# Performance work log

Measured on AMD Instinct MI355X. Metric: run time of the kernel, lower is better.

## Reference

```python
import jax, jax.numpy as jnp
import numpy as np

N = 32768   # nodes
E = 32768   # edges
ND, ED, GD = 12, 5, 11
H = 64
T = 4
STEPS = 3


def setup_inputs() -> dict:
    key = jax.random.key(0)
    ks = jax.random.split(key, 24)
    s = 0.05
    p = lambda k, sh: (jax.random.normal(k, sh) * s).astype(jnp.float32)
    return dict(
        x=jax.random.normal(ks[0], (N, ND), jnp.float32),
        edge_index=jax.random.randint(ks[1], (2, E), 0, N, jnp.int64),
        edge_attr=jax.random.uniform(ks[2], (E, ED), jnp.float32),
        u=jax.random.normal(ks[3], (1, GD), jnp.float32),
        Wp=p(ks[4], (H, ND + GD)), bp=p(ks[5], (H,)),
        We1=p(ks[6], (H, ED)), be1=p(ks[7], (H,)),
        We2=p(ks[8], (H * H, H)), be2=p(ks[9], (H * H,)),
        root=p(ks[10], (H, H)), conv_b=p(ks[11], (H,)),
        Wih=p(ks[12], (3 * H, H)), bih=p(ks[13], (3 * H,)),
        Whh=p(ks[14], (3 * H, H)), bhh=p(ks[15], (3 * H,)),
        Wd1=p(ks[16], (H, 2 * H + ED)), bd1=p(ks[17], (H,)),
        Wd2=p(ks[18], (H // 2, H)), bd2=p(ks[19], (H // 2,)),
        Wd3=p(ks[20], (T, H // 2)), bd3=p(ks[21], (T,)),
    )


def _forward(x, edge_index, edge_attr, u,
             Wp, bp, We1, be1, We2, be2, root, conv_b,
             Wih, bih, Whh, bhh, Wd1, bd1, Wd2, bd2, Wd3, bd3):
    n = x.shape[0]
    e = edge_attr.shape[0]
    src, dst = edge_index[0], edge_index[1]

    # input projection with broadcast global features (batch=None path)
    u_node = jnp.broadcast_to(u, (n, u.shape[-1]))
    h = jnp.tanh(jnp.concatenate([x, u_node], axis=-1) @ Wp.T + bp)

    # edge MLP -> per-edge (H,H) weight matrices; edge_attr is loop-invariant
    ew = jax.nn.relu(edge_attr @ We1.T + be1) @ We2.T + be2   # (E, H*H)
    ew = ew.reshape(e, H, H)                                   # (E, H, H)

    # mean-aggregation denominators (clamped to 1 like scatter-mean)
    counts = jnp.clip(jax.ops.segment_sum(jnp.ones((e,), h.dtype), dst, num_segments=n), 1.0)

    for _ in range(STEPS):
        # NNConv: gather src features, per-edge matmul, scatter-mean into dst
        msg = jnp.einsum('eh,eho->eo', h[src], ew)             # (E, H)
        agg = jax.ops.segment_sum(msg, dst, num_segments=n) / counts[:, None]
        m = jax.nn.relu(agg + h @ root + conv_b)               # dropout off (eval)
        # GRUCell (torch gate order: r, z, n)
        gi = m @ Wih.T + bih
        gh = h @ Whh.T + bhh
        r = jax.nn.sigmoid(gi[:, :H] + gh[:, :H])
        z = jax.nn.sigmoid(gi[:, H:2 * H] + gh[:, H:2 * H])
        ng = jnp.tanh(gi[:, 2 * H:] + r * gh[:, 2 * H:])
        h = (1.0 - z) * ng + z * h

    # per-edge decoder
    e_in = jnp.concatenate([h[src], h[dst], edge_attr], axis=-1)
    d = jax.nn.relu(e_in @ Wd1.T + bd1)
    d = jax.nn.relu(d @ Wd2.T + bd2)
    return d @ Wd3.T + bd3                                     # (E, T)


def reference(x, edge_index, edge_attr, u,
              Wp, bp, We1, be1, We2, be2, root, conv_b,
              Wih, bih, Whh, bhh, Wd1, bd1, Wd2, bd2, Wd3, bd3):
    return _forward(x, edge_index, edge_attr, u,
                    Wp, bp, We1, be1, We2, be2, root, conv_b,
                    Wih, bih, Whh, bhh, Wd1, bd1, Wd2, bd2, Wd3, bd3)
```

## Files before the change

kernel.cpp:

```cpp
#include <hip/hip_runtime.h>
#include <hip/hip_bf16.h>
#include <stdint.h>


#define N_NODES 32768
#define N_EDGES 32768
#define STEPS 3

typedef __attribute__((ext_vector_type(8))) short short8;
typedef __attribute__((ext_vector_type(4))) float float4v;

__device__ __forceinline__ float bf2f(unsigned short u) {
    union { unsigned int i; float f; } v; v.i = ((unsigned int)u) << 16; return v.f;
}
__device__ __forceinline__ unsigned short f2bf(float f) {
    union { float f; unsigned int i; } v; v.f = f;
    unsigned int x = v.i;
    return (unsigned short)((x + 0x7fffu + ((x >> 16) & 1u)) >> 16);
}
__device__ __forceinline__ unsigned int fbits(float f) {
    union { float f; unsigned int i; } v; v.f = f; return v.i;
}

__device__ __forceinline__ short8 packA(float hv, const float* hf) {
    union { short8 v; unsigned int u[4]; } r;
#pragma unroll
    for (int p = 0; p < 4; p++) {
        unsigned int p0 = fbits(hv * hf[2 * p]) + 0x8000u;
        unsigned int p1 = fbits(hv * hf[2 * p + 1]) + 0x8000u;
        r.u[p] = __builtin_amdgcn_perm(p1, p0, 0x07060302u);
    }
    return r.v;
}

__device__ __forceinline__ void gload_lds16(const void* g, void* l) {
    __builtin_amdgcn_global_load_lds(
        (__attribute__((address_space(1))) void*)g,
        (__attribute__((address_space(3))) void*)l, 16, 0, 0);
}

__global__ __launch_bounds__(256) void k_setup(
    const float* __restrict__ root, const float* __restrict__ Wih,
    const float* __restrict__ Whh,
    const float* __restrict__ We2, const float* __restrict__ be2,
    const float* __restrict__ Wd1, const float* __restrict__ bd1,
    const float* __restrict__ Wd2,
    const float* __restrict__ x, const float* __restrict__ u,
    const float* __restrict__ Wp, const float* __restrict__ bp,
    const float* __restrict__ ea, const float* __restrict__ We1,
    const float* __restrict__ be1,
    unsigned short* __restrict__ rootTf, unsigned short* __restrict__ wcombf,
    unsigned short* __restrict__ w2tf,
    unsigned short* __restrict__ wd1f, unsigned short* __restrict__ wd2f,
    unsigned short* __restrict__ hb,
    unsigned short* __restrict__ hid, float* __restrict__ aggcnt)
{
    int b = blockIdx.x, tid = threadIdx.x;
    if (b < 144) {
        int i = b * 256 + tid;
        if (i < 4096) {
            int j = i & 7, lane = (i >> 3) & 63, g = i >> 9;
            int kb = g >> 2, nf = g & 3;
            int o = nf * 16 + (lane & 15);
            int k = kb * 32 + (lane >> 4) * 8 + j;
            rootTf[i] = f2bf(root[k * 64 + o]);
        } else if (i < 4096 + 32768) {
            int t = i - 4096;
            int j = t & 7, lane = (t >> 3) & 63, g = t >> 9;
            int kb = g >> 4, nf = g & 15;
            int cp = nf * 16 + (lane & 15);
            int k = kb * 32 + (lane >> 4) * 8 + j;
            float v;
            if (cp < 128)      v = (k < 64) ? Wih[cp * 64 + k] : Whh[cp * 64 + (k - 64)];
            else if (cp < 192) v = (k < 64) ? Wih[cp * 64 + k] : 0.f;
            else               v = (k < 64) ? 0.f : Whh[(cp - 64) * 64 + (k - 64)];
            wcombf[t] = f2bf(v);
        }
    } else if (b < 1184) {
        int t = (b - 144) * 256 + tid;
        if (t < 65 * 4096) {
            int kk = t >> 12, r = t & 4095;
            int j = r & 7, lane = (r >> 3) & 63, g = r >> 9;
            int half = g >> 2, nf = g & 3;
            int o = nf * 16 + (lane & 15);
            int hh = half * 32 + (lane >> 4) * 8 + j;
            float v = (kk < 64) ? We2[((size_t)(hh * 64 + o)) * 64 + kk]
                                : be2[(size_t)hh * 64 + o];
            w2tf[t] = f2bf(v);
        }
    } else if (b < 1232) {
        int i = (b - 1184) * 256 + tid;
        if (i < 10240) {
            int j = i & 7, lane = (i >> 3) & 63, g = i >> 9;
            int kb = g >> 2, nf = g & 3;
            int o = nf * 16 + (lane & 15);
            int k = kb * 32 + (lane >> 4) * 8 + j;
            float v = (k < 133) ? Wd1[(size_t)o * 133 + k] : (k == 133 ? bd1[o] : 0.f);
            wd1f[i] = f2bf(v);
        } else if (i < 10240 + 2048) {
            int t = i - 10240;
            int j = t & 7, lane = (t >> 3) & 63, g = t >> 9;
            int kb = g >> 1, nf = g & 1;
            int o = nf * 16 + (lane & 15);
            int k = kb * 32 + (lane >> 4) * 8 + j;
            wd2f[t] = f2bf(Wd2[(size_t)o * 64 + k]);
        }
    } else if (b < 9424) {
        int idx = (b - 1232) * 256 + tid;
        int n = idx >> 6, j = idx & 63;
        const float* wr = Wp + j * 23;
        const float* xr = x + (size_t)n * 12;
        float s = bp[j];
#pragma unroll
        for (int i = 0; i < 12; i++) s += xr[i] * wr[i];
#pragma unroll
        for (int i = 0; i < 11; i++) s += u[i] * wr[12 + i];
        hb[idx] = f2bf(tanhf(s));
    } else if (b < 17616) {
        int idx = (b - 9424) * 256 + tid;
        int e = idx >> 6, j = idx & 63;
        float s = be1[j];
#pragma unroll
        for (int i = 0; i < 5; i++) s += ea[(size_t)e * 5 + i] * We1[j * 5 + i];
        hid[idx] = f2bf(s > 0.f ? s : 0.f);
    } else {
        int idx = (b - 17616) * 1024 + tid * 4;
        if (idx < 2129920) {
            float4v z = {0.f, 0.f, 0.f, 0.f};
            *(float4v*)(aggcnt + idx) = z;
        }
    }
}

__global__ __launch_bounds__(256) void k_counts(
    const int* __restrict__ ei, float* __restrict__ counts)
{
    int i = blockIdx.x * 256 + threadIdx.x;
    if (i < N_EDGES) atomicAdd(&counts[ei[N_EDGES + i]], 1.0f);
}

__global__ __launch_bounds__(512, 4) void k_msg_fused(
    const unsigned short* __restrict__ hid,
    const unsigned short* __restrict__ hb,
    const unsigned short* __restrict__ w2tf,
    const int* __restrict__ ei,
    float* __restrict__ agg)
{
    __shared__ unsigned short buf[2][2][8192];
    int tid = threadIdx.x, wave = tid >> 6, lane = tid & 63;
    int l15 = lane & 15, quad = lane >> 4;
    int mf = wave & 3, kh = wave >> 2;
    int ebase = blockIdx.x * 64 + mf * 16;
    int e_a = ebase + l15;
    int src = ei[e_a];

    union { short8 v[4]; unsigned short u[32]; } hrow;
#pragma unroll
    for (int i = 0; i < 4; i++)
        hrow.v[i] = *(const short8*)(hid + (size_t)e_a * 64 + kh * 32 + i * 8);

    float hf0[8], hf1[8];
    {
        short8 h0 = *(const short8*)(hb + (size_t)src * 64 + quad * 8);
        short8 h1 = *(const short8*)(hb + (size_t)src * 64 + 32 + quad * 8);
#pragma unroll
        for (int j = 0; j < 8; j++) {
            hf0[j] = bf2f((unsigned short)h0[j]);
            hf1[j] = bf2f((unsigned short)h1[j]);
        }
    }

    int kk0 = kh ? 32 : 0;
    auto stage = [&](int pair, int db) {
        const unsigned short* g = w2tf + (size_t)(kk0 + 2 * pair) * 4096;
#pragma unroll
        for (int c = 0; c < 4; c++) {
            int chunk = mf * 4 + c;
            gload_lds16(g + (size_t)chunk * 512 + lane * 8, &buf[kh][db][chunk * 512]);
        }
    };

    stage(0, 0);

    float4v acc[4] = {};
    int cur = 0;
#pragma unroll
    for (int i = 0; i <= 16; i++) {
        __syncthreads();
        if ((kh == 0 && i + 1 < 16) || (kh == 1 && i + 1 <= 16))
            stage(i + 1, cur ^ 1);
        int nkk = (kh == 0) ? (i < 16 ? 2 : 0) : (i < 16 ? 2 : 1);
        for (int s = 0; s < nkk; s++) {
            float hv = (kh == 1 && i == 16) ? 1.0f : bf2f(hrow.u[2 * i + s]);
            short8 a0 = packA(hv, hf0);
            short8 a1 = packA(hv, hf1);
            const unsigned short* bp = &buf[kh][cur][s * 4096];
#pragma unroll
            for (int nf = 0; nf < 4; nf++) {
                short8 b0 = *(const short8*)(bp + (0 * 4 + nf) * 512 + lane * 8);
                acc[nf] = __builtin_amdgcn_mfma_f32_16x16x32_bf16(a0, b0, acc[nf], 0, 0, 0);
            }
#pragma unroll
            for (int nf = 0; nf < 4; nf++) {
                short8 b1 = *(const short8*)(bp + (1 * 4 + nf) * 512 + lane * 8);
                acc[nf] = __builtin_amdgcn_mfma_f32_16x16x32_bf16(a1, b1, acc[nf], 0, 0, 0);
            }
        }
        cur ^= 1;
    }

    __syncthreads();
    float* mg = (float*)&buf[0][0][0];
    if (kh == 1) {
#pragma unroll
        for (int nf = 0; nf < 4; nf++)
#pragma unroll
            for (int r = 0; r < 4; r++)
                mg[mf * 1024 + lane * 16 + nf * 4 + r] = acc[nf][r];
    }
    __syncthreads();
    if (kh == 0) {
        int dsts[4];
#pragma unroll
        for (int r = 0; r < 4; r++) dsts[r] = ei[N_EDGES + ebase + quad * 4 + r];
#pragma unroll
        for (int nf = 0; nf < 4; nf++)
#pragma unroll
            for (int r = 0; r < 4; r++)
                atomicAdd(agg + (size_t)dsts[r] * 64 + nf * 16 + l15,
                          acc[nf][r] + mg[mf * 1024 + lane * 16 + nf * 4 + r]);
    }
}

__global__ __launch_bounds__(256) void k_node(
    const unsigned short* __restrict__ hb_in,
    const unsigned short* __restrict__ rootTf,
    const unsigned short* __restrict__ wcombf,
    float* __restrict__ agg, const float* __restrict__ counts,
    const float* __restrict__ conv_b,
    const float* __restrict__ bih, const float* __restrict__ bhh,
    unsigned short* __restrict__ hb_out)
{
    __shared__ unsigned short m_lds[64 * 72];
    int tid = threadIdx.x, w = tid >> 6, lane = tid & 63;
    int l15 = lane & 15, quad = lane >> 4;
    int node0 = blockIdx.x * 64;
    int row0 = w * 16;

    float4v acc1[4] = {};
    {
        short8 a1[2];
#pragma unroll
        for (int kb = 0; kb < 2; kb++)
            a1[kb] = *(const short8*)(hb_in + (size_t)(node0 + row0 + l15) * 64 + kb * 32 + quad * 8);
#pragma unroll
        for (int kb = 0; kb < 2; kb++)
#pragma unroll
            for (int nf = 0; nf < 4; nf++) {
                short8 b = *(const short8*)(rootTf + (size_t)((kb * 4 + nf) * 64 + lane) * 8);
                acc1[nf] = __builtin_amdgcn_mfma_f32_16x16x32_bf16(a1[kb], b, acc1[nf], 0, 0, 0);
            }
    }
#pragma unroll
    for (int rr = 0; rr < 4; rr++) {
        int nl = row0 + quad * 4 + rr;
        float cnt = counts[node0 + nl]; if (cnt < 1.f) cnt = 1.f;
        float rcp = 1.f / cnt;
#pragma unroll
        for (int nf = 0; nf < 4; nf++) {
            int c = nf * 16 + l15;
            float* ap = agg + (size_t)(node0 + nl) * 64 + c;
            float av = *ap;
            *ap = 0.f;
            float mv = av * rcp + acc1[nf][rr] + conv_b[c];
            m_lds[nl * 72 + c] = f2bf(mv > 0.f ? mv : 0.f);
        }
    }
    __syncthreads();

    float4v acc2[16] = {};
#pragma unroll
    for (int kb = 0; kb < 4; kb++) {
        short8 a2;
        if (kb < 2)
            a2 = *(const short8*)(m_lds + (row0 + l15) * 72 + kb * 32 + quad * 8);
        else
            a2 = *(const short8*)(hb_in + (size_t)(node0 + row0 + l15) * 64 + (kb - 2) * 32 + quad * 8);
#pragma unroll
        for (int nf = 0; nf < 16; nf++) {
            short8 b = *(const short8*)(wcombf + (size_t)((kb * 16 + nf) * 64 + lane) * 8);
            acc2[nf] = __builtin_amdgcn_mfma_f32_16x16x32_bf16(a2, b, acc2[nf], 0, 0, 0);
        }
    }

#pragma unroll
    for (int nf0 = 0; nf0 < 4; nf0++) {
        int c = nf0 * 16 + l15;
        float br = bih[c] + bhh[c];
        float bz = bih[64 + c] + bhh[64 + c];
        float bni = bih[128 + c], bnh = bhh[128 + c];
#pragma unroll
        for (int rr = 0; rr < 4; rr++) {
            int node = node0 + row0 + quad * 4 + rr;
            float gr = 1.f / (1.f + __expf(-(acc2[nf0][rr] + br)));
            float gz = 1.f / (1.f + __expf(-(acc2[nf0 + 4][rr] + bz)));
            float ng = tanhf(acc2[nf0 + 8][rr] + bni + gr * (acc2[nf0 + 12][rr] + bnh));
            float ho = bf2f(hb_in[(size_t)node * 64 + c]);
            float hn = (1.f - gz) * ng + gz * ho;
            hb_out[(size_t)node * 64 + c] = f2bf(hn);
        }
    }
}

__global__ __launch_bounds__(256) void k_decoder(
    const unsigned short* __restrict__ hb, const int* __restrict__ ei,
    const float* __restrict__ ea,
    const unsigned short* __restrict__ wd1f, const unsigned short* __restrict__ wd2f,
    const float* __restrict__ bd2,
    const float* __restrict__ Wd3, const float* __restrict__ bd3,
    float* __restrict__ out)
{
    __shared__ unsigned short d1f[4][1024];
    __shared__ float d2s[4][16 * 33];
    int tid = threadIdx.x, w = tid >> 6, lane = tid & 63;
    int l15 = lane & 15, quad = lane >> 4;
    int ebase = blockIdx.x * 64 + w * 16;
    int e = ebase + l15;
    int src = ei[e], dst = ei[N_EDGES + e];

    short8 a[5];
#pragma unroll
    for (int kb = 0; kb < 2; kb++) {
        a[kb]     = *(const short8*)(hb + (size_t)src * 64 + kb * 32 + quad * 8);
        a[2 + kb] = *(const short8*)(hb + (size_t)dst * 64 + kb * 32 + quad * 8);
    }
    {
        union { short8 v; unsigned short u[8]; } tea;
#pragma unroll
        for (int j = 0; j < 8; j++) {
            float vv = 0.f;
            if (quad == 0) vv = (j < 5) ? ea[(size_t)e * 5 + j] : (j == 5 ? 1.f : 0.f);
            tea.u[j] = f2bf(vv);
        }
        a[4] = tea.v;
    }

    float4v acc1[4] = {};
#pragma unroll
    for (int kb = 0; kb < 5; kb++)
#pragma unroll
        for (int nf = 0; nf < 4; nf++) {
            short8 b = *(const short8*)(wd1f + (size_t)((kb * 4 + nf) * 64 + lane) * 8);
            acc1[nf] = __builtin_amdgcn_mfma_f32_16x16x32_bf16(a[kb], b, acc1[nf], 0, 0, 0);
        }
#pragma unroll
    for (int nf = 0; nf < 4; nf++) {
        int kbp = nf >> 1;
        int lanep_hi = ((nf & 1) * 2 + (l15 >> 3)) * 16;
        int jp = l15 & 7;
#pragma unroll
        for (int r = 0; r < 4; r++) {
            float v = acc1[nf][r];
            d1f[w][kbp * 512 + (lanep_hi + quad * 4 + r) * 8 + jp] = f2bf(v > 0.f ? v : 0.f);
        }
    }
    float4v acc2[2] = {};
#pragma unroll
    for (int kb = 0; kb < 2; kb++) {
        short8 a2 = *(const short8*)(&d1f[w][kb * 512 + lane * 8]);
#pragma unroll
        for (int nf = 0; nf < 2; nf++) {
            short8 b = *(const short8*)(wd2f + (size_t)((kb * 2 + nf) * 64 + lane) * 8);
            acc2[nf] = __builtin_amdgcn_mfma_f32_16x16x32_bf16(a2, b, acc2[nf], 0, 0, 0);
        }
    }
#pragma unroll
    for (int nf = 0; nf < 2; nf++) {
        int c = nf * 16 + l15;
        float bias = bd2[c];
#pragma unroll
        for (int r = 0; r < 4; r++) {
            float v = acc2[nf][r] + bias;
            d2s[w][(quad * 4 + r) * 33 + c] = v > 0.f ? v : 0.f;
        }
    }
    {
        int e_l = lane >> 2, t = lane & 3;
        float s = bd3[t];
        const float* w3 = Wd3 + t * 32;
        const float* dr = &d2s[w][e_l * 33];
#pragma unroll
        for (int k = 0; k < 32; k++) s += w3[k] * dr[k];
        out[(size_t)(ebase + e_l) * 4 + t] = s;
    }
}

extern "C" void kernel_launch(void* const* d_in, const int* in_sizes, int n_in,
                              void* d_out, int out_size, void* d_ws, size_t ws_size,
                              hipStream_t stream)
{
    const float* x      = (const float*)d_in[0];
    const int*   ei     = (const int*)d_in[1];
    const float* ea     = (const float*)d_in[2];
    const float* u      = (const float*)d_in[3];
    const float* Wp     = (const float*)d_in[4];
    const float* bp     = (const float*)d_in[5];
    const float* We1    = (const float*)d_in[6];
    const float* be1    = (const float*)d_in[7];
    const float* We2    = (const float*)d_in[8];
    const float* be2    = (const float*)d_in[9];
    const float* root   = (const float*)d_in[10];
    const float* conv_b = (const float*)d_in[11];
    const float* Wih    = (const float*)d_in[12];
    const float* bih    = (const float*)d_in[13];
    const float* Whh    = (const float*)d_in[14];
    const float* bhh    = (const float*)d_in[15];
    const float* Wd1    = (const float*)d_in[16];
    const float* bd1    = (const float*)d_in[17];
    const float* Wd2    = (const float*)d_in[18];
    const float* bd2    = (const float*)d_in[19];
    const float* Wd3    = (const float*)d_in[20];
    const float* bd3    = (const float*)d_in[21];
    float* out = (float*)d_out;

    char* ws = (char*)d_ws;
    size_t off = 0;
    auto take = [&](size_t bytes) -> char* {
        char* p = ws + off; off = (off + bytes + 255) & ~(size_t)255; return p;
    };
    unsigned short* hb     = (unsigned short*)take((size_t)N_NODES * 64 * 2);
    unsigned short* hid    = (unsigned short*)take((size_t)N_EDGES * 64 * 2);
    float*          aggcnt = (float*)take((size_t)(N_NODES * 64 + N_NODES) * 4);
    float*          agg    = aggcnt;
    float*          cnts   = aggcnt + (size_t)N_NODES * 64;
    unsigned short* w2tf   = (unsigned short*)take((size_t)66 * 4096 * 2);
    unsigned short* rootTf = (unsigned short*)take((size_t)4096 * 2);
    unsigned short* wcombf = (unsigned short*)take((size_t)32768 * 2);
    unsigned short* wd1f   = (unsigned short*)take((size_t)10240 * 2);
    unsigned short* wd2f   = (unsigned short*)take((size_t)2048 * 2);
    (void)ws_size;

    k_setup<<<19696, 256, 0, stream>>>(root, Wih, Whh, We2, be2, Wd1, bd1, Wd2,
                                       x, u, Wp, bp, ea, We1, be1,
                                       rootTf, wcombf, w2tf, wd1f, wd2f,
                                       hb, hid, aggcnt);
    k_counts<<<128, 256, 0, stream>>>(ei, cnts);

    for (int s = 0; s < STEPS; s++) {
        k_msg_fused<<<N_EDGES / 64, 512, 0, stream>>>(hid, hb, w2tf, ei, agg);
        k_node<<<N_NODES / 64, 256, 0, stream>>>(hb, rootTf, wcombf, agg, cnts,
                                                 conv_b, bih, bhh, hb);
    }
    k_decoder<<<N_EDGES / 64, 256, 0, stream>>>(hb, ei, ea, wd1f, wd2f, bd2,
                                                Wd3, bd3, out);
}
```

Baseline: 267.0 us.

## Fuse counts, message steps, node updates and decoder into one cooperative kernel

Replaces the separate counts, per-step message, node-update and decoder launches with one persistent cooperative kernel of 256 blocks. Grid-wide syncs separate the phases. Each block now handles 128 edges or nodes, and each wave processes two 16-edge fragments that share the staged edge-weight tiles. This cuts kernel launch gaps and halves weight staging per edge. In exchange, only one 512-thread block runs per CU, which lowers occupancy and latency hiding, and each step adds grid-sync costs.

After: 981.0 us. 267% more time.

```diff
diff --git a/kernel.cpp b/kernel.cpp
--- a/kernel.cpp
+++ b/kernel.cpp
@@ -1,4 +1,5 @@
 #include <hip/hip_runtime.h>
+#include <hip/hip_cooperative_groups.h>
 #include <hip/hip_bf16.h>
 #include <stdint.h>
 
@@ -6,6 +7,8 @@
 #define N_NODES 32768
 #define N_EDGES 32768
 #define STEPS 3
+
+namespace cg = cooperative_groups;
 
 typedef __attribute__((ext_vector_type(8))) short short8;
 typedef __attribute__((ext_vector_type(4))) float float4v;
@@ -132,266 +135,277 @@
     }
 }
 
-__global__ __launch_bounds__(256) void k_counts(
-    const int* __restrict__ ei, float* __restrict__ counts)
-{
-    int i = blockIdx.x * 256 + threadIdx.x;
-    if (i < N_EDGES) atomicAdd(&counts[ei[N_EDGES + i]], 1.0f);
-}
-
-__global__ __launch_bounds__(512, 4) void k_msg_fused(
+__global__ __launch_bounds__(512, 2) void k_main(
     const unsigned short* __restrict__ hid,
-    const unsigned short* __restrict__ hb,
+    unsigned short* __restrict__ hb,
     const unsigned short* __restrict__ w2tf,
     const int* __restrict__ ei,
-    float* __restrict__ agg)
-{
-    __shared__ unsigned short buf[2][2][8192];
-    int tid = threadIdx.x, wave = tid >> 6, lane = tid & 63;
-    int l15 = lane & 15, quad = lane >> 4;
-    int mf = wave & 3, kh = wave >> 2;
-    int ebase = blockIdx.x * 64 + mf * 16;
-    int e_a = ebase + l15;
-    int src = ei[e_a];
-
-    union { short8 v[4]; unsigned short u[32]; } hrow;
-#pragma unroll
-    for (int i = 0; i < 4; i++)
-        hrow.v[i] = *(const short8*)(hid + (size_t)e_a * 64 + kh * 32 + i * 8);
-
-    float hf0[8], hf1[8];
-    {
-        short8 h0 = *(const short8*)(hb + (size_t)src * 64 + quad * 8);
-        short8 h1 = *(const short8*)(hb + (size_t)src * 64 + 32 + quad * 8);
-#pragma unroll
-        for (int j = 0; j < 8; j++) {
-            hf0[j] = bf2f((unsigned short)h0[j]);
-            hf1[j] = bf2f((unsigned short)h1[j]);
-        }
-    }
-
-    int kk0 = kh ? 32 : 0;
-    auto stage = [&](int pair, int db) {
-        const unsigned short* g = w2tf + (size_t)(kk0 + 2 * pair) * 4096;
-#pragma unroll
-        for (int c = 0; c < 4; c++) {
-            int chunk = mf * 4 + c;
-            gload_lds16(g + (size_t)chunk * 512 + lane * 8, &buf[kh][db][chunk * 512]);
-        }
-    };
-
-    stage(0, 0);
-
-    float4v acc[4] = {};
-    int cur = 0;
-#pragma unroll
-    for (int i = 0; i <= 16; i++) {
-        __syncthreads();
-        if ((kh == 0 && i + 1 < 16) || (kh == 1 && i + 1 <= 16))
-            stage(i + 1, cur ^ 1);
-        int nkk = (kh == 0) ? (i < 16 ? 2 : 0) : (i < 16 ? 2 : 1);
-        for (int s = 0; s < nkk; s++) {
-            float hv = (kh == 1 && i == 16) ? 1.0f : bf2f(hrow.u[2 * i + s]);
-            short8 a0 = packA(hv, hf0);
-            short8 a1 = packA(hv, hf1);
-            const unsigned short* bp = &buf[kh][cur][s * 4096];
-#pragma unroll
-            for (int nf = 0; nf < 4; nf++) {
-                short8 b0 = *(const short8*)(bp + (0 * 4 + nf) * 512 + lane * 8);
-                acc[nf] = __builtin_amdgcn_mfma_f32_16x16x32_bf16(a0, b0, acc[nf], 0, 0, 0);
-            }
-#pragma unroll
-            for (int nf = 0; nf < 4; nf++) {
-                short8 b1 = *(const short8*)(bp + (1 * 4 + nf) * 512 + lane * 8);
-                acc[nf] = __builtin_amdgcn_mfma_f32_16x16x32_bf16(a1, b1, acc[nf], 0, 0, 0);
-            }
-        }
-        cur ^= 1;
-    }
-
-    __syncthreads();
-    float* mg = (float*)&buf[0][0][0];
-    if (kh == 1) {
-#pragma unroll
-        for (int nf = 0; nf < 4; nf++)
-#pragma unroll
-            for (int r = 0; r < 4; r++)
-                mg[mf * 1024 + lane * 16 + nf * 4 + r] = acc[nf][r];
-    }
-    __syncthreads();
-    if (kh == 0) {
-        int dsts[4];
-#pragma unroll
-        for (int r = 0; r < 4; r++) dsts[r] = ei[N_EDGES + ebase + quad * 4 + r];
-#pragma unroll
-        for (int nf = 0; nf < 4; nf++)
-#pragma unroll
-            for (int r = 0; r < 4; r++)
-                atomicAdd(agg + (size_t)dsts[r] * 64 + nf * 16 + l15,
-                          acc[nf][r] + mg[mf * 1024 + lane * 16 + nf * 4 + r]);
-    }
-}
-
-__global__ __launch_bounds__(256) void k_node(
-    const unsigned short* __restrict__ hb_in,
+    float* __restrict__ agg, float* __restrict__ cnts,
     const unsigned short* __restrict__ rootTf,
     const unsigned short* __restrict__ wcombf,
-    float* __restrict__ agg, const float* __restrict__ counts,
     const float* __restrict__ conv_b,
     const float* __restrict__ bih, const float* __restrict__ bhh,
-    unsigned short* __restrict__ hb_out)
-{
-    __shared__ unsigned short m_lds[64 * 72];
-    int tid = threadIdx.x, w = tid >> 6, lane = tid & 63;
-    int l15 = lane & 15, quad = lane >> 4;
-    int node0 = blockIdx.x * 64;
-    int row0 = w * 16;
-
-    float4v acc1[4] = {};
-    {
-        short8 a1[2];
-#pragma unroll
-        for (int kb = 0; kb < 2; kb++)
-            a1[kb] = *(const short8*)(hb_in + (size_t)(node0 + row0 + l15) * 64 + kb * 32 + quad * 8);
-#pragma unroll
-        for (int kb = 0; kb < 2; kb++)
-#pragma unroll
-            for (int nf = 0; nf < 4; nf++) {
-                short8 b = *(const short8*)(rootTf + (size_t)((kb * 4 + nf) * 64 + lane) * 8);
-                acc1[nf] = __builtin_amdgcn_mfma_f32_16x16x32_bf16(a1[kb], b, acc1[nf], 0, 0, 0);
-            }
-    }
-#pragma unroll
-    for (int rr = 0; rr < 4; rr++) {
-        int nl = row0 + quad * 4 + rr;
-        float cnt = counts[node0 + nl]; if (cnt < 1.f) cnt = 1.f;
-        float rcp = 1.f / cnt;
-#pragma unroll
-        for (int nf = 0; nf < 4; nf++) {
-            int c = nf * 16 + l15;
-            float* ap = agg + (size_t)(node0 + nl) * 64 + c;
-            float av = *ap;
-            *ap = 0.f;
-            float mv = av * rcp + acc1[nf][rr] + conv_b[c];
-            m_lds[nl * 72 + c] = f2bf(mv > 0.f ? mv : 0.f);
-        }
-    }
-    __syncthreads();
-
-    float4v acc2[16] = {};
-#pragma unroll
-    for (int kb = 0; kb < 4; kb++) {
-        short8 a2;
-        if (kb < 2)
-            a2 = *(const short8*)(m_lds + (row0 + l15) * 72 + kb * 32 + quad * 8);
-        else
-            a2 = *(const short8*)(hb_in + (size_t)(node0 + row0 + l15) * 64 + (kb - 2) * 32 + quad * 8);
-#pragma unroll
-        for (int nf = 0; nf < 16; nf++) {
-            short8 b = *(const short8*)(wcombf + (size_t)((kb * 16 + nf) * 64 + lane) * 8);
-            acc2[nf] = __builtin_amdgcn_mfma_f32_16x16x32_bf16(a2, b, acc2[nf], 0, 0, 0);
-        }
-    }
-
-#pragma unroll
-    for (int nf0 = 0; nf0 < 4; nf0++) {
-        int c = nf0 * 16 + l15;
-        float br = bih[c] + bhh[c];
-        float bz = bih[64 + c] + bhh[64 + c];
-        float bni = bih[128 + c], bnh = bhh[128 + c];
-#pragma unroll
-        for (int rr = 0; rr < 4; rr++) {
-            int node = node0 + row0 + quad * 4 + rr;
-            float gr = 1.f / (1.f + __expf(-(acc2[nf0][rr] + br)));
-            float gz = 1.f / (1.f + __expf(-(acc2[nf0 + 4][rr] + bz)));
-            float ng = tanhf(acc2[nf0 + 8][rr] + bni + gr * (acc2[nf0 + 12][rr] + bnh));
-            float ho = bf2f(hb_in[(size_t)node * 64 + c]);
-            float hn = (1.f - gz) * ng + gz * ho;
-            hb_out[(size_t)node * 64 + c] = f2bf(hn);
-        }
-    }
-}
-
-__global__ __launch_bounds__(256) void k_decoder(
-    const unsigned short* __restrict__ hb, const int* __restrict__ ei,
     const float* __restrict__ ea,
-    const unsigned short* __restrict__ wd1f, const unsigned short* __restrict__ wd2f,
+    const unsigned short* __restrict__ wd1f,
+    const unsigned short* __restrict__ wd2f,
     const float* __restrict__ bd2,
     const float* __restrict__ Wd3, const float* __restrict__ bd3,
     float* __restrict__ out)
 {
-    __shared__ unsigned short d1f[4][1024];
-    __shared__ float d2s[4][16 * 33];
-    int tid = threadIdx.x, w = tid >> 6, lane = tid & 63;
+    cg::grid_group grid = cg::this_grid();
+    __shared__ unsigned short smem[2][2][8192];
+    int tid = threadIdx.x, wave = tid >> 6, lane = tid & 63;
     int l15 = lane & 15, quad = lane >> 4;
-    int ebase = blockIdx.x * 64 + w * 16;
-    int e = ebase + l15;
-    int src = ei[e], dst = ei[N_EDGES + e];
-
-    short8 a[5];
-#pragma unroll
-    for (int kb = 0; kb < 2; kb++) {
-        a[kb]     = *(const short8*)(hb + (size_t)src * 64 + kb * 32 + quad * 8);
-        a[2 + kb] = *(const short8*)(hb + (size_t)dst * 64 + kb * 32 + quad * 8);
+
+    {
+        int gtid = blockIdx.x * 512 + tid;
+        if (gtid < N_EDGES) atomicAdd(&cnts[ei[N_EDGES + gtid]], 1.0f);
     }
+
+    for (int step = 0; step < STEPS; step++) {
+        {
+            int mf = wave & 3, kh = wave >> 2;
+            int ebase = blockIdx.x * 128 + mf * 32;
+            int src0 = ei[ebase + l15], src1 = ei[ebase + 16 + l15];
+
+            union Hrow { short8 v[4]; unsigned short u[32]; };
+            Hrow hrow[2];
+#pragma unroll
+            for (int i = 0; i < 4; i++) {
+                hrow[0].v[i] = *(const short8*)(hid + (size_t)(ebase + l15) * 64 + kh * 32 + i * 8);
+                hrow[1].v[i] = *(const short8*)(hid + (size_t)(ebase + 16 + l15) * 64 + kh * 32 + i * 8);
+            }
+            float hf[2][2][8];
+#pragma unroll
+            for (int f = 0; f < 2; f++) {
+                int src = f ? src1 : src0;
+                short8 h0 = *(const short8*)(hb + (size_t)src * 64 + quad * 8);
+                short8 h1 = *(const short8*)(hb + (size_t)src * 64 + 32 + quad * 8);
+#pragma unroll
+                for (int j = 0; j < 8; j++) {
+                    hf[f][0][j] = bf2f((unsigned short)h0[j]);
+                    hf[f][1][j] = bf2f((unsigned short)h1[j]);
+                }
+            }
+
+            int kk0 = kh ? 32 : 0;
+            auto stage = [&](int pair, int db) {
+                const unsigned short* g = w2tf + (size_t)(kk0 + 2 * pair) * 4096;
+#pragma unroll
+                for (int c = 0; c < 4; c++) {
+                    int chunk = mf * 4 + c;
+                    gload_lds16(g + (size_t)chunk * 512 + lane * 8, &smem[kh][db][chunk * 512]);
+                }
+            };
+            stage(0, 0);
+
+            float4v acc[2][4] = {};
+            int cur = 0;
+#pragma unroll
+            for (int i = 0; i <= 16; i++) {
+                __syncthreads();
+                if ((kh == 0 && i + 1 < 16) || (kh == 1 && i + 1 <= 16))
+                    stage(i + 1, cur ^ 1);
+                int nkk = (kh == 0) ? (i < 16 ? 2 : 0) : (i < 16 ? 2 : 1);
+                for (int s = 0; s < nkk; s++) {
+                    const unsigned short* bp = &smem[kh][cur][s * 4096];
+                    short8 b0[4], b1[4];
+#pragma unroll
+                    for (int nf = 0; nf < 4; nf++) {
+                        b0[nf] = *(const short8*)(bp + (0 * 4 + nf) * 512 + lane * 8);
+                        b1[nf] = *(const short8*)(bp + (1 * 4 + nf) * 512 + lane * 8);
+                    }
+#pragma unroll
+                    for (int f = 0; f < 2; f++) {
+                        float hv = (kh == 1 && i == 16) ? 1.0f : bf2f(hrow[f].u[2 * i + s]);
+                        short8 a0 = packA(hv, hf[f][0]);
+                        short8 a1 = packA(hv, hf[f][1]);
+#pragma unroll
+                        for (int nf = 0; nf < 4; nf++)
+                            acc[f][nf] = __builtin_amdgcn_mfma_f32_16x16x32_bf16(a0, b0[nf], acc[f][nf], 0, 0, 0);
+#pragma unroll
+                        for (int nf = 0; nf < 4; nf++)
+                            acc[f][nf] = __builtin_amdgcn_mfma_f32_16x16x32_bf16(a1, b1[nf], acc[f][nf], 0, 0, 0);
+                    }
+                }
+                cur ^= 1;
+            }
+
+            __syncthreads();
+            float* mg = (float*)&smem[0][0][0];
+            if (kh == 1) {
+#pragma unroll
+                for (int f = 0; f < 2; f++)
+#pragma unroll
+                    for (int nf = 0; nf < 4; nf++)
+#pragma unroll
+                        for (int r = 0; r < 4; r++)
+                            mg[(mf * 2 + f) * 1024 + lane * 16 + nf * 4 + r] = acc[f][nf][r];
+            }
+            __syncthreads();
+            if (kh == 0) {
+#pragma unroll
+                for (int f = 0; f < 2; f++) {
+                    int dsts[4];
+#pragma unroll
+                    for (int r = 0; r < 4; r++)
+                        dsts[r] = ei[N_EDGES + ebase + f * 16 + quad * 4 + r];
+#pragma unroll
+                    for (int nf = 0; nf < 4; nf++)
+#pragma unroll
+                        for (int r = 0; r < 4; r++)
+                            atomicAdd(agg + (size_t)dsts[r] * 64 + nf * 16 + l15,
+                                      acc[f][nf][r] + mg[(mf * 2 + f) * 1024 + lane * 16 + nf * 4 + r]);
+                }
+            }
+        }
+        __threadfence();
+        grid.sync();
+
+        {
+            unsigned short* m_lds = (unsigned short*)&smem[0][0][0];
+            int node0 = blockIdx.x * 128;
+            int row0 = wave * 16;
+
+            float4v acc1[4] = {};
+            {
+                short8 a1[2];
+#pragma unroll
+                for (int kb = 0; kb < 2; kb++)
+                    a1[kb] = *(const short8*)(hb + (size_t)(node0 + row0 + l15) * 64 + kb * 32 + quad * 8);
+#pragma unroll
+                for (int kb = 0; kb < 2; kb++)
+#pragma unroll
+                    for (int nf = 0; nf < 4; nf++) {
+                        short8 b = *(const short8*)(rootTf + (size_t)((kb * 4 + nf) * 64 + lane) * 8);
+                        acc1[nf] = __builtin_amdgcn_mfma_f32_16x16x32_bf16(a1[kb], b, acc1[nf], 0, 0, 0);
+                    }
+            }
+#pragma unroll
+            for (int rr = 0; rr < 4; rr++) {
+                int nl = row0 + quad * 4 + rr;
+                float cnt = cnts[node0 + nl]; if (cnt < 1.f) cnt = 1.f;
+                float rcp = 1.f / cnt;
+#pragma unroll
+                for (int nf = 0; nf < 4; nf++) {
+                    int c = nf * 16 + l15;
+                    float* ap = agg + (size_t)(node0 + nl) * 64 + c;
+                    float av = *ap;
+                    *ap = 0.f;
+                    float mv = av * rcp + acc1[nf][rr] + conv_b[c];
+                    m_lds[nl * 72 + c] = f2bf(mv > 0.f ? mv : 0.f);
+                }
+            }
+            __syncthreads();
+
+            float4v acc2[16] = {};
+#pragma unroll
+            for (int kb = 0; kb < 4; kb++) {
+                short8 a2;
+                if (kb < 2)
+                    a2 = *(const short8*)(m_lds + (row0 + l15) * 72 + kb * 32 + quad * 8);
+                else
+                    a2 = *(const short8*)(hb + (size_t)(node0 + row0 + l15) * 64 + (kb - 2) * 32 + quad * 8);
+#pragma unroll
+                for (int nf = 0; nf < 16; nf++) {
+                    short8 b = *(const short8*)(wcombf + (size_t)((kb * 16 + nf) * 64 + lane) * 8);
+                    acc2[nf] = __builtin_amdgcn_mfma_f32_16x16x32_bf16(a2, b, acc2[nf], 0, 0, 0);
+                }
+            }
+#pragma unroll
+            for (int nf0 = 0; nf0 < 4; nf0++) {
+                int c = nf0 * 16 + l15;
+                float br = bih[c] + bhh[c];
+                float bz = bih[64 + c] + bhh[64 + c];
+                float bni = bih[128 + c], bnh = bhh[128 + c];
+#pragma unroll
+                for (int rr = 0; rr < 4; rr++) {
+                    int node = node0 + row0 + quad * 4 + rr;
+                    float gr = 1.f / (1.f + __expf(-(acc2[nf0][rr] + br)));
+                    float gz = 1.f / (1.f + __expf(-(acc2[nf0 + 4][rr] + bz)));
+                    float ng = tanhf(acc2[nf0 + 8][rr] + bni + gr * (acc2[nf0 + 12][rr] + bnh));
+                    float ho = bf2f(hb[(size_t)node * 64 + c]);
+                    float hn = (1.f - gz) * ng + gz * ho;
+                    hb[(size_t)node * 64 + c] = f2bf(hn);
+                }
+            }
+        }
+        __threadfence();
+        grid.sync();
+    }
+
     {
-        union { short8 v; unsigned short u[8]; } tea;
-#pragma unroll
-        for (int j = 0; j < 8; j++) {
-            float vv = 0.f;
-            if (quad == 0) vv = (j < 5) ? ea[(size_t)e * 5 + j] : (j == 5 ? 1.f : 0.f);
-            tea.u[j] = f2bf(vv);
-        }
-        a[4] = tea.v;
-    }
-
-    float4v acc1[4] = {};
-#pragma unroll
-    for (int kb = 0; kb < 5; kb++)
+        unsigned short* d1f = (unsigned short*)&smem[0][0][0];
+        float* d2s = (float*)((char*)&smem[0][0][0] + 16384);
+        int ebase = blockIdx.x * 128 + wave * 16;
+        int e = ebase + l15;
+        int src = ei[e], dst = ei[N_EDGES + e];
+
+        short8 a[5];
+#pragma unroll
+        for (int kb = 0; kb < 2; kb++) {
+            a[kb]     = *(const short8*)(hb + (size_t)src * 64 + kb * 32 + quad * 8);
+            a[2 + kb] = *(const short8*)(hb + (size_t)dst * 64 + kb * 32 + quad * 8);
+        }
+        {
+            union { short8 v; unsigned short u[8]; } tea;
+#pragma unroll
+            for (int j = 0; j < 8; j++) {
+                float vv = 0.f;
+                if (quad == 0) vv = (j < 5) ? ea[(size_t)e * 5 + j] : (j == 5 ? 1.f : 0.f);
+                tea.u[j] = f2bf(vv);
+            }
+            a[4] = tea.v;
+        }
+
+        float4v acc1[4] = {};
+#pragma unroll
+        for (int kb = 0; kb < 5; kb++)
+#pragma unroll
+            for (int nf = 0; nf < 4; nf++) {
+                short8 b = *(const short8*)(wd1f + (size_t)((kb * 4 + nf) * 64 + lane) * 8);
+                acc1[nf] = __builtin_amdgcn_mfma_f32_16x16x32_bf16(a[kb], b, acc1[nf], 0, 0, 0);
+            }
 #pragma unroll
         for (int nf = 0; nf < 4; nf++) {
-            short8 b = *(const short8*)(wd1f + (size_t)((kb * 4 + nf) * 64 + lane) * 8);
-            acc1[nf] = __builtin_amdgcn_mfma_f32_16x16x32_bf16(a[kb], b, acc1[nf], 0, 0, 0);
-        }
-#pragma unroll
-    for (int nf = 0; nf < 4; nf++) {
-        int kbp = nf >> 1;
-        int lanep_hi = ((nf & 1) * 2 + (l15 >> 3)) * 16;
-        int jp = l15 & 7;
-#pragma unroll
-        for (int r = 0; r < 4; r++) {
-            float v = acc1[nf][r];
-            d1f[w][kbp * 512 + (lanep_hi + quad * 4 + r) * 8 + jp] = f2bf(v > 0.f ? v : 0.f);
-        }
-    }
-    float4v acc2[2] = {};
-#pragma unroll
-    for (int kb = 0; kb < 2; kb++) {
-        short8 a2 = *(const short8*)(&d1f[w][kb * 512 + lane * 8]);
+            int kbp = nf >> 1;
+            int lanep_hi = ((nf & 1) * 2 + (l15 >> 3)) * 16;
+            int jp = l15 & 7;
+#pragma unroll
+            for (int r = 0; r < 4; r++) {
+                float v = acc1[nf][r];
+                d1f[wave * 1024 + kbp * 512 + (lanep_hi + quad * 4 + r) * 8 + jp] = f2bf(v > 0.f ? v : 0.f);
+            }
+        }
+        float4v acc2[2] = {};
+#pragma unroll
+        for (int kb = 0; kb < 2; kb++) {
+            short8 a2 = *(const short8*)(&d1f[wave * 1024 + kb * 512 + lane * 8]);
+#pragma unroll
+            for (int nf = 0; nf < 2; nf++) {
+                short8 b = *(const short8*)(wd2f + (size_t)((kb * 2 + nf) * 64 + lane) * 8);
+                acc2[nf] = __builtin_amdgcn_mfma_f32_16x16x32_bf16(a2, b, acc2[nf], 0, 0, 0);
+            }
+        }
 #pragma unroll
         for (int nf = 0; nf < 2; nf++) {
-            short8 b = *(const short8*)(wd2f + (size_t)((kb * 2 + nf) * 64 + lane) * 8);
-            acc2[nf] = __builtin_amdgcn_mfma_f32_16x16x32_bf16(a2, b, acc2[nf], 0, 0, 0);
-        }
-    }
-#pragma unroll
-    for (int nf = 0; nf < 2; nf++) {
-        int c = nf * 16 + l15;
-        float bias = bd2[c];
-#pragma unroll
-        for (int r = 0; r < 4; r++) {
-            float v = acc2[nf][r] + bias;
-            d2s[w][(quad * 4 + r) * 33 + c] = v > 0.f ? v : 0.f;
-        }
-    }
-    {
-        int e_l = lane >> 2, t = lane & 3;
-        float s = bd3[t];
-        const float* w3 = Wd3 + t * 32;
-        const float* dr = &d2s[w][e_l * 33];
-#pragma unroll
-        for (int k = 0; k < 32; k++) s += w3[k] * dr[k];
-        out[(size_t)(ebase + e_l) * 4 + t] = s;
+            int c = nf * 16 + l15;
+            float bias = bd2[c];
+#pragma unroll
+            for (int r = 0; r < 4; r++) {
+                float v = acc2[nf][r] + bias;
+                d2s[wave * 528 + (quad * 4 + r) * 33 + c] = v > 0.f ? v : 0.f;
+            }
+        }
+        {
+            int e_l = lane >> 2, t = lane & 3;
+            float s = bd3[t];
+            const float* w3 = Wd3 + t * 32;
+            const float* dr = &d2s[wave * 528 + e_l * 33];
+#pragma unroll
+            for (int k = 0; k < 32; k++) s += w3[k] * dr[k];
+            out[(size_t)(ebase + e_l) * 4 + t] = s;
+        }
     }
 }
 
@@ -444,13 +458,14 @@
                                        x, u, Wp, bp, ea, We1, be1,
                                        rootTf, wcombf, w2tf, wd1f, wd2f,
                                        hb, hid, aggcnt);
-    k_counts<<<128, 256, 0, stream>>>(ei, cnts);
-
-    for (int s = 0; s < STEPS; s++) {
-        k_msg_fused<<<N_EDGES / 64, 512, 0, stream>>>(hid, hb, w2tf, ei, agg);
-        k_node<<<N_NODES / 64, 256, 0, stream>>>(hb, rootTf, wcombf, agg, cnts,
-                                                 conv_b, bih, bhh, hb);
-    }
-    k_decoder<<<N_EDGES / 64, 256, 0, stream>>>(hb, ei, ea, wd1f, wd2f, bd2,
-                                                Wd3, bd3, out);
-}
+
+    void* args[] = {
+        (void*)&hid, (void*)&hb, (void*)&w2tf, (void*)&ei,
+        (void*)&agg, (void*)&cnts, (void*)&rootTf, (void*)&wcombf,
+        (void*)&conv_b, (void*)&bih, (void*)&bhh, (void*)&ea,
+        (void*)&wd1f, (void*)&wd2f, (void*)&bd2,
+        (void*)&Wd3, (void*)&bd3, (void*)&out
+    };
+    hipLaunchCooperativeKernel((const void*)k_main, dim3(256), dim3(512),
+                               args, 0, stream);
+}
```

## Give each message wave two 16-edge tiles to reuse staged weight fragments

Applied to the files above, without the earlier changes.

The message kernel drops from 8 waves to 4 per block, and each wave now computes two 16-edge M-fragments. Each LDS-loaded B fragment of the edge-network weight therefore feeds twice as many MFMAs, halving LDS read traffic per MFMA. Each wave also stages twice as many weight chunks. The partial-sum exchange buffer is padded with stride 17 to reduce bank conflicts. The cost is more registers per wave (two accumulator sets, more h buffers) and fewer waves per block, which may reduce latency hiding; the main k loop is also no longer fully unrolled.

After: 332.8 us. 1.25x slower.

```diff
diff --git a/kernel.cpp b/kernel.cpp
--- a/kernel.cpp
+++ b/kernel.cpp
@@ -139,7 +139,7 @@
     if (i < N_EDGES) atomicAdd(&counts[ei[N_EDGES + i]], 1.0f);
 }
 
-__global__ __launch_bounds__(512, 4) void k_msg_fused(
+__global__ __launch_bounds__(256) void k_msg_fused(
     const unsigned short* __restrict__ hid,
     const unsigned short* __restrict__ hb,
     const unsigned short* __restrict__ w2tf,
@@ -149,24 +149,25 @@
     __shared__ unsigned short buf[2][2][8192];
     int tid = threadIdx.x, wave = tid >> 6, lane = tid & 63;
     int l15 = lane & 15, quad = lane >> 4;
-    int mf = wave & 3, kh = wave >> 2;
-    int ebase = blockIdx.x * 64 + mf * 16;
-    int e_a = ebase + l15;
-    int src = ei[e_a];
-
-    union { short8 v[4]; unsigned short u[32]; } hrow;
-#pragma unroll
-    for (int i = 0; i < 4; i++)
-        hrow.v[i] = *(const short8*)(hid + (size_t)e_a * 64 + kh * 32 + i * 8);
-
-    float hf0[8], hf1[8];
-    {
+    int mf = wave & 1, kh = wave >> 1;
+    int ebase = blockIdx.x * 64 + mf * 32;
+
+    union Hrow { short8 v[4]; unsigned short u[32]; };
+    Hrow hrow[2];
+    float hf[2][2][8];
+#pragma unroll
+    for (int f = 0; f < 2; f++) {
+        int e_a = ebase + f * 16 + l15;
+#pragma unroll
+        for (int i = 0; i < 4; i++)
+            hrow[f].v[i] = *(const short8*)(hid + (size_t)e_a * 64 + kh * 32 + i * 8);
+        int src = ei[e_a];
         short8 h0 = *(const short8*)(hb + (size_t)src * 64 + quad * 8);
         short8 h1 = *(const short8*)(hb + (size_t)src * 64 + 32 + quad * 8);
 #pragma unroll
         for (int j = 0; j < 8; j++) {
-            hf0[j] = bf2f((unsigned short)h0[j]);
-            hf1[j] = bf2f((unsigned short)h1[j]);
+            hf[f][0][j] = bf2f((unsigned short)h0[j]);
+            hf[f][1][j] = bf2f((unsigned short)h1[j]);
         }
     }
 
@@ -174,36 +175,39 @@
     auto stage = [&](int pair, int db) {
         const unsigned short* g = w2tf + (size_t)(kk0 + 2 * pair) * 4096;
 #pragma unroll
-        for (int c = 0; c < 4; c++) {
-            int chunk = mf * 4 + c;
+        for (int c = 0; c < 8; c++) {
+            int chunk = mf * 8 + c;
             gload_lds16(g + (size_t)chunk * 512 + lane * 8, &buf[kh][db][chunk * 512]);
         }
     };
-
     stage(0, 0);
 
-    float4v acc[4] = {};
+    float4v acc[2][4] = {};
     int cur = 0;
-#pragma unroll
     for (int i = 0; i <= 16; i++) {
         __syncthreads();
         if ((kh == 0 && i + 1 < 16) || (kh == 1 && i + 1 <= 16))
             stage(i + 1, cur ^ 1);
         int nkk = (kh == 0) ? (i < 16 ? 2 : 0) : (i < 16 ? 2 : 1);
         for (int s = 0; s < nkk; s++) {
-            float hv = (kh == 1 && i == 16) ? 1.0f : bf2f(hrow.u[2 * i + s]);
-            short8 a0 = packA(hv, hf0);
-            short8 a1 = packA(hv, hf1);
             const unsigned short* bp = &buf[kh][cur][s * 4096];
+            short8 b0[4], b1[4];
 #pragma unroll
             for (int nf = 0; nf < 4; nf++) {
-                short8 b0 = *(const short8*)(bp + (0 * 4 + nf) * 512 + lane * 8);
-                acc[nf] = __builtin_amdgcn_mfma_f32_16x16x32_bf16(a0, b0, acc[nf], 0, 0, 0);
+                b0[nf] = *(const short8*)(bp + (0 * 4 + nf) * 512 + lane * 8);
+                b1[nf] = *(const short8*)(bp + (1 * 4 + nf) * 512 + lane * 8);
             }
 #pragma unroll
-            for (int nf = 0; nf < 4; nf++) {
-                short8 b1 = *(const short8*)(bp + (1 * 4 + nf) * 512 + lane * 8);
-                acc[nf] = __builtin_amdgcn_mfma_f32_16x16x32_bf16(a1, b1, acc[nf], 0, 0, 0);
+            for (int f = 0; f < 2; f++) {
+                float hv = (kh == 1 && i == 16) ? 1.0f : bf2f(hrow[f].u[(2 * i + s) & 31]);
+                short8 a0 = packA(hv, hf[f][0]);
+                short8 a1 = packA(hv, hf[f][1]);
+#pragma unroll
+                for (int nf = 0; nf < 4; nf++)
+                    acc[f][nf] = __builtin_amdgcn_mfma_f32_16x16x32_bf16(a0, b0[nf], acc[f][nf], 0, 0, 0);
+#pragma unroll
+                for (int nf = 0; nf < 4; nf++)
+                    acc[f][nf] = __builtin_amdgcn_mfma_f32_16x16x32_bf16(a1, b1[nf], acc[f][nf], 0, 0, 0);
             }
         }
         cur ^= 1;
@@ -213,22 +217,28 @@
     float* mg = (float*)&buf[0][0][0];
     if (kh == 1) {
 #pragma unroll
-        for (int nf = 0; nf < 4; nf++)
-#pragma unroll
-            for (int r = 0; r < 4; r++)
-                mg[mf * 1024 + lane * 16 + nf * 4 + r] = acc[nf][r];
+        for (int f = 0; f < 2; f++)
+#pragma unroll
+            for (int nf = 0; nf < 4; nf++)
+#pragma unroll
+                for (int r = 0; r < 4; r++)
+                    mg[((mf * 2 + f) * 64 + lane) * 17 + nf * 4 + r] = acc[f][nf][r];
     }
     __syncthreads();
     if (kh == 0) {
-        int dsts[4];
-#pragma unroll
-        for (int r = 0; r < 4; r++) dsts[r] = ei[N_EDGES + ebase + quad * 4 + r];
-#pragma unroll
-        for (int nf = 0; nf < 4; nf++)
+#pragma unroll
+        for (int f = 0; f < 2; f++) {
+            int dsts[4];
 #pragma unroll
             for (int r = 0; r < 4; r++)
-                atomicAdd(agg + (size_t)dsts[r] * 64 + nf * 16 + l15,
-                          acc[nf][r] + mg[mf * 1024 + lane * 16 + nf * 4 + r]);
+                dsts[r] = ei[N_EDGES + ebase + f * 16 + quad * 4 + r];
+#pragma unroll
+            for (int nf = 0; nf < 4; nf++)
+#pragma unroll
+                for (int r = 0; r < 4; r++)
+                    atomicAdd(agg + (size_t)dsts[r] * 64 + nf * 16 + l15,
+                              acc[f][nf][r] + mg[((mf * 2 + f) * 64 + lane) * 17 + nf * 4 + r]);
+        }
     }
 }
 
@@ -447,7 +457,7 @@
     k_counts<<<128, 256, 0, stream>>>(ei, cnts);
 
     for (int s = 0; s < STEPS; s++) {
-        k_msg_fused<<<N_EDGES / 64, 512, 0, stream>>>(hid, hb, w2tf, ei, agg);
+        k_msg_fused<<<N_EDGES / 64, 256, 0, stream>>>(hid, hb, w2tf, ei, agg);
         k_node<<<N_NODES / 64, 256, 0, stream>>>(hb, rootTf, wcombf, agg, cnts,
                                                  conv_b, bih, bhh, hb);
     }
```
